# Performance work log

Measured on AMD Instinct MI355X. Metric: run time of the kernel, lower is better.

The kernel has to match this reference:

```python
import jax, jax.numpy as jnp
import numpy as np

BATCH, D_IN, D_HIDDEN, K = 4096, 2048, 16384, 64


def setup_inputs() -> dict:
    key = jax.random.key(0)
    kx, kw = jax.random.split(key)
    x = jax.random.normal(kx, (BATCH, D_IN), dtype=jnp.float32)
    # W init as in the module: randn normalized per column (dim=0) then scaled by 0.1
    W = jax.random.normal(kw, (D_IN, D_HIDDEN), dtype=jnp.float32)
    W = 0.1 * W / jnp.linalg.norm(W, axis=0, keepdims=True)
    b_enc = jnp.zeros((D_HIDDEN,), dtype=jnp.float32)
    b_dec = jnp.zeros((D_IN,), dtype=jnp.float32)
    return {"x": x, "W": W, "b_enc": b_enc, "b_dec": b_dec, "k": K}


def reference(x, W, b_enc, b_dec, k):
    # encode: linear + ReLU
    f = jax.nn.relu(x @ W + b_enc)            # [B, D_HIDDEN]
    # global batch top-k: keep k * batch largest activations across the whole batch
    flat = f.reshape(-1)                      # [B * D_HIDDEN]
    n_keep = k * x.shape[0]                   # static python int
    vals, idx = jax.lax.top_k(flat, n_keep)
    f_topk = jnp.zeros_like(flat).at[idx].set(vals).reshape(f.shape)
    # tied decode
    recon = f_topk @ W.T + b_dec              # [B, D_IN]
    return (recon, f_topk)
```

## Files before the change

### kernel.cpp

```cpp
#include <hip/hip_runtime.h>
#include <stdint.h>


#define BATCH 4096
#define DIN   2048
#define DHID  16384
#define NELEM (BATCH * DHID)
#define RECON_ELEMS (BATCH * DIN)
#define NBINS 8192
#define THRESH_BIN 1664
#define SC_THRESH 0.203125f
#define WIN   3
#define RLCAP 256
#define CBUF2 512
#define NB2 (NBINS - THRESH_BIN)
#define NB2H (NB2 / 2)
#define SCHUNK 32
#define NCH ((NB2 + SCHUNK - 1) / SCHUNK)
#define NKT 32
#define SBUF8 4096
#define WSCALE_INV 0.00390625f

#define XB_OFF   0u
#define HIST_OFF 16777216u
#define META_OFF (HIST_OFF + 32768u)
#define CAND_OFF (HIST_OFF + 65536u)
#define CANDCAP  80000u
#define SC_OFF   18874368u
#define SCCAP    1835008u

#define M_CNT   0
#define M_BLO   1
#define M_BHI   2
#define M_NNEED 3
#define M_NSURE 4
#define M_OVF   5
#define M_SCCNT 6

struct Cand { unsigned long long key; unsigned int idx; float val; };

typedef _Float16 f16x8 __attribute__((ext_vector_type(8)));
typedef float f32x4  __attribute__((ext_vector_type(4)));

__device__ __forceinline__ int binof(float v) {
    int b = (int)(v * 8192.0f);
    return b > (NBINS - 1) ? (NBINS - 1) : b;
}

__device__ __forceinline__ unsigned short f2h(float f) {
    _Float16 h = (_Float16)f;
    return __builtin_bit_cast(unsigned short, h);
}

__device__ __forceinline__ float h2f(unsigned short u) {
    return (float)__builtin_bit_cast(_Float16, u);
}

__device__ __forceinline__ void gload_lds16(const void* g, void* l) {
    __builtin_amdgcn_global_load_lds(
        (const __attribute__((address_space(1))) void*)g,
        (__attribute__((address_space(3))) void*)l, 16, 0, 0);
}

__device__ __forceinline__ void nt_store4(const float4& v, float* p) {
    f32x4 x = {v.x, v.y, v.z, v.w};
    __builtin_nontemporal_store(x, (f32x4*)p);
}

__global__ void init_kernel(unsigned* __restrict__ hist, unsigned* __restrict__ meta) {
    int i = blockIdx.x * 256 + threadIdx.x;
    if (i < NBINS) hist[i] = 0u;
    if (i < 64)    meta[i] = 0u;
}

__global__ __launch_bounds__(256) void prep_kernel(const float* __restrict__ X,
                                                   unsigned short* __restrict__ Xh,
                                                   const float* __restrict__ W,
                                                   float* __restrict__ WT,
                                                   unsigned short* __restrict__ WhT,
                                                   unsigned* __restrict__ hist,
                                                   unsigned* __restrict__ meta,
                                                   unsigned* __restrict__ rowcnt) {
    __shared__ float tile[64][68];
    const int bid = blockIdx.x;
    const int t   = threadIdx.x;
    if (bid < 8192) {
        size_t i = (size_t)bid * 256 + t;
        float4 v = ((const float4*)X)[i];
        ushort4 o;
        o.x = f2h(v.x); o.y = f2h(v.y); o.z = f2h(v.z); o.w = f2h(v.w);
        ((ushort4*)Xh)[i] = o;
        if (bid < 32) {
            int g = bid * 256 + t;
            if (g < NBINS)  hist[g] = 0u;
            if (g < 64)     meta[g] = 0u;
            if (g < BATCH)  rowcnt[g] = 0u;
        }
        return;
    }
    const int bb = bid - 8192;
    const int gx = bb & 255;
    const int gy = bb >> 8;
    const int ra = t >> 4;
    const int ca = (t & 15) * 4;
#pragma unroll
    for (int u = 0; u < 4; ++u) {
        int row = u * 16 + ra;
        float4 v = *(const float4*)&W[(size_t)(gy * 64 + row) * DHID + gx * 64 + ca];
        tile[ca + 0][row] = v.x;
        tile[ca + 1][row] = v.y;
        tile[ca + 2][row] = v.z;
        tile[ca + 3][row] = v.w;
    }
    __syncthreads();
#pragma unroll
    for (int u = 0; u < 4; ++u) {
        int cl = u * 16 + ra;
        float4 v = *(const float4*)&tile[cl][ca];
        size_t o = (size_t)(gx * 64 + cl) * DIN + gy * 64 + ca;
        *(float4*)&WT[o] = v;
        ushort4 b;
        b.x = f2h(v.x * 256.0f); b.y = f2h(v.y * 256.0f);
        b.z = f2h(v.z * 256.0f); b.w = f2h(v.w * 256.0f);
        *(ushort4*)&WhT[o] = b;
    }
}


#define STAGE_A(H, KT) do { if ((KT) < NKT) {                                   \
    const unsigned short* _s = Xh + (size_t)(m0 + (H)*128 + stgrow)*2048        \
                               + (KT)*64 + stgcol;                              \
    unsigned short* _d = lds + ((H)*2 + ((KT)&1))*8192 + stgdst;                \
    gload_lds16(_s, _d);                                                        \
    gload_lds16(_s + 64*2048, _d + 4096);                                       \
} } while (0)

#define STAGE_B(H, KT) do { if ((KT) < NKT) {                                   \
    const unsigned short* _s = WhT + (size_t)(n0 + (H)*128 + stgrow)*2048       \
                               + (KT)*64 + stgcol;                              \
    unsigned short* _d = lds + 32768 + ((H)*2 + ((KT)&1))*8192 + stgdst;        \
    gload_lds16(_s, _d);                                                        \
    gload_lds16(_s + 64*2048, _d + 4096);                                       \
} } while (0)

#define LDA(DST, AH, PAR) do {                                                  \
    _Pragma("unroll")                                                           \
    for (int i = 0; i < 4; ++i) {                                               \
        const unsigned short* _p = lds + ((AH)*2+(PAR))*8192                    \
                                   + (wr2*64 + i*16 + lm)*64;                   \
        DST[i][0] = *(const f16x8*)(_p + cs0);                                  \
        DST[i][1] = *(const f16x8*)(_p + cs1);                                  \
    }                                                                           \
} while (0)

#define LDB(DST, BH, PAR) do {                                                  \
    _Pragma("unroll")                                                           \
    for (int j = 0; j < 2; ++j) {                                               \
        const unsigned short* _p = lds + 32768 + ((BH)*2+(PAR))*8192            \
                                   + (wn*32 + j*16 + lm)*64;                    \
        DST[j][0] = *(const f16x8*)(_p + cs0);                                  \
        DST[j][1] = *(const f16x8*)(_p + cs1);                                  \
    }                                                                           \
} while (0)

#define DO_MFMA(Q, AV, BV) do {                                                 \
    __builtin_amdgcn_s_barrier();                                               \
    asm volatile("s_waitcnt lgkmcnt(0)" ::: "memory");                          \
    __builtin_amdgcn_sched_barrier(0);                                          \
    __builtin_amdgcn_s_setprio(1);                                              \
    _Pragma("unroll")                                                           \
    for (int i = 0; i < 4; ++i)                                                 \
    _Pragma("unroll")                                                           \
    for (int j = 0; j < 2; ++j) {                                               \
        acc[Q][i][j] = __builtin_amdgcn_mfma_f32_16x16x32_f16(                  \
            AV[i][0], BV[j][0], acc[Q][i][j], 0, 0, 0);                         \
        acc[Q][i][j] = __builtin_amdgcn_mfma_f32_16x16x32_f16(                  \
            AV[i][1], BV[j][1], acc[Q][i][j], 0, 0, 0);                         \
    }                                                                           \
    __builtin_amdgcn_s_setprio(0);                                              \
    __builtin_amdgcn_s_barrier();                                               \
    asm volatile("" ::: "memory");                                              \
} while (0)

#define TILE_BODY(PAR, T) do {                                                  \
    LDA(av, 0, PAR); LDB(bv0, 0, PAR);                                          \
    STAGE_B(0, (T) + 1); STAGE_A(1, (T) + 1);                                   \
    DO_MFMA(0, av, bv0);                                                        \
    LDB(bv1, 1, PAR);                                                           \
    DO_MFMA(1, av, bv1);                                                        \
    LDA(av, 1, PAR);                                                            \
    STAGE_A(0, (T) + 2);                                                        \
    DO_MFMA(2, av, bv1);                                                        \
    STAGE_B(1, (T) + 2);                                                        \
    asm volatile("s_waitcnt vmcnt(4)" ::: "memory");                            \
    DO_MFMA(3, av, bv0);                                                        \
} while (0)

__global__ __launch_bounds__(512, 2) void encode_mfma8(const unsigned short* __restrict__ Xh,
                                                       const unsigned short* __restrict__ WhT,
                                                       const float* __restrict__ benc,
                                                       unsigned long long* __restrict__ sc,
                                                       unsigned* __restrict__ meta,
                                                       unsigned* __restrict__ hist,
                                                       float* __restrict__ F) {
    __shared__ unsigned short lds[65536];
    __shared__ unsigned hsh[NB2H];
    __shared__ unsigned s_n, s_base;

    const int t   = threadIdx.x;
    const int wid = t >> 6;
    const int l   = t & 63;
    const int wr2 = wid >> 2;
    const int wn  = wid & 3;
    const int lm  = l & 15;
    const int l7  = l & 7;
    const int cs0 = ((l >> 4) * 8) ^ (l7 * 8);
    const int cs1 = cs0 ^ 32;
    const int stgrow = wid * 8 + (l >> 3);
    const int stgcol = (l7 ^ (l >> 3)) * 8;
    const int stgdst = wid * 512;

    if (t == 0) s_n = 0u;
    for (int i2 = t; i2 < NB2H; i2 += 512) hsh[i2] = 0u;

    const unsigned id  = blockIdx.x;
    const unsigned xcd = id & 7u;
    const unsigned c   = id >> 3;
    const int bx = (int)(xcd * 8u + (c & 7u));
    const int by = (int)(c >> 3);
    const int m0 = by * 256;
    const int n0 = bx * 256;

    f32x4 acc[4][4][2];
#pragma unroll
    for (int q = 0; q < 4; ++q)
#pragma unroll
        for (int i = 0; i < 4; ++i)
#pragma unroll
            for (int j = 0; j < 2; ++j) acc[q][i][j] = (f32x4){0.f, 0.f, 0.f, 0.f};

    STAGE_A(0, 0); STAGE_B(0, 0); STAGE_B(1, 0); STAGE_A(1, 0);
    STAGE_A(0, 1); STAGE_B(1, 1);
    asm volatile("s_waitcnt vmcnt(4)" ::: "memory");
    __builtin_amdgcn_s_barrier();
    asm volatile("" ::: "memory");

    {
        f16x8 av[4][2], bv0[2][2], bv1[2][2];
#pragma unroll 1
        for (int it = 0; it < 16; ++it) {
            const int T = 2 * it;
            TILE_BODY(0, T);
            TILE_BODY(1, T + 1);
        }
    }

    __syncthreads();
    unsigned long long* sbuf = (unsigned long long*)lds;

#pragma unroll
    for (int q = 0; q < 4; ++q) {
        const int qm = (q >= 2) ? 1 : 0;
        const int qn = (q == 1 || q == 2) ? 1 : 0;
#pragma unroll
        for (int j = 0; j < 2; ++j) {
            const int col = n0 + qn * 128 + wn * 32 + j * 16 + lm;
            const float bias = benc[col];
#pragma unroll
            for (int i = 0; i < 4; ++i) {
                const int rbase = m0 + qm * 128 + wr2 * 64 + i * 16 + (l >> 4) * 4;
#pragma unroll
                for (int r = 0; r < 4; ++r) {
                    float v = fmaxf(acc[q][i][j][r] * WSCALE_INV + bias, 0.0f);
                    if (v >= SC_THRESH) {
                        unsigned hx = (unsigned)(binof(v) - THRESH_BIN);
                        atomicAdd(&hsh[hx >> 1], (hx & 1u) ? 65536u : 1u);
                        unsigned flat = (unsigned)(rbase + r) * (unsigned)DHID + (unsigned)col;
                        unsigned long long e =
                            ((unsigned long long)__float_as_uint(v) << 32) | flat;
                        unsigned pos = atomicAdd(&s_n, 1u);
                        if (pos < SBUF8) sbuf[pos] = e;
                        else {
                            unsigned p = atomicAdd(&meta[M_SCCNT], 1u);
                            if (p < SCCAP) sc[p] = e; else meta[M_OVF] = 1u;
                        }
                    }
                }
            }
        }
    }
    {
        const float4 z4 = {0.f, 0.f, 0.f, 0.f};
        const int zr = t >> 6;
        const int zc = (t & 63) * 4;
#pragma unroll 1
        for (int rr = 0; rr < 32; ++rr)
            nt_store4(z4, &F[(size_t)(m0 + zr + rr * 8) * DHID + n0 + zc]);
    }
    __syncthreads();
    unsigned n = s_n < SBUF8 ? s_n : (unsigned)SBUF8;
    if (t == 0) s_base = atomicAdd(&meta[M_SCCNT], n);
    __syncthreads();
    const unsigned base = s_base;
    for (unsigned l2 = t; l2 < n; l2 += 512) {
        unsigned p = base + l2;
        if (p < SCCAP) sc[p] = sbuf[l2]; else meta[M_OVF] = 1u;
    }
    for (int i2 = t; i2 < NB2H; i2 += 512) {
        unsigned u = hsh[i2];
        unsigned lo = u & 0xFFFFu, hi = u >> 16;
        if (lo) atomicAdd(&hist[THRESH_BIN + 2 * i2], lo);
        if (hi) atomicAdd(&hist[THRESH_BIN + 2 * i2 + 1], hi);
    }
}

__global__ void scan_sc(const unsigned* __restrict__ hist,
                        unsigned* __restrict__ meta,
                        const int* __restrict__ kptr) {
    __shared__ unsigned sh[NB2];
    __shared__ unsigned csum[NCH];
    int t = threadIdx.x;
    for (int i = t; i < NB2; i += 256) sh[i] = hist[THRESH_BIN + i];
    __syncthreads();
    if (t < NCH) {
        unsigned s = 0;
        int base = t * SCHUNK;
        for (int u = 0; u < SCHUNK && base + u < NB2; ++u) s += sh[base + u];
        csum[t] = s;
    }
    __syncthreads();
    if (t == 0) {
        unsigned nk = (unsigned)kptr[0] * BATCH;
        unsigned cum = 0;
        int bstar_idx = -1;
        for (int c = NCH - 1; c >= 0; --c) {
            if (cum + csum[c] >= nk) {
                int hi2 = c * SCHUNK + SCHUNK - 1; if (hi2 >= NB2) hi2 = NB2 - 1;
                for (int idx = hi2; idx >= c * SCHUNK; --idx) {
                    cum += sh[idx];
                    if (cum >= nk) { bstar_idx = idx; break; }
                }
                break;
            } else cum += csum[c];
        }
        if (bstar_idx < 0) { meta[M_OVF] = 2u; bstar_idx = WIN; }
        int bstar = THRESH_BIN + bstar_idx;
        int blo = bstar - WIN;
        if (blo < THRESH_BIN) { meta[M_OVF] = 3u; blo = THRESH_BIN; }
        int bhi = bstar + WIN; if (bhi > NBINS - 1) bhi = NBINS - 1;
        int bhi_idx = bhi - THRESH_BIN;
        unsigned nsure = 0;
        int cstart = (bhi_idx + 1 + SCHUNK - 1) / SCHUNK;
        for (int idx = bhi_idx + 1; idx < cstart * SCHUNK && idx < NB2; ++idx) nsure += sh[idx];
        for (int c = cstart; c < NCH; ++c) nsure += csum[c];
        meta[M_BLO]   = (unsigned)blo;
        meta[M_BHI]   = (unsigned)bhi;
        meta[M_NSURE] = nsure;
        meta[M_NNEED] = nk - nsure;
    }
}

__global__ __launch_bounds__(256) void emit_sc(const unsigned long long* __restrict__ sc,
                                               unsigned* __restrict__ meta,
                                               Cand* __restrict__ cand,
                                               unsigned* __restrict__ rowcnt,
                                               unsigned long long* __restrict__ rowlist,
                                               float* __restrict__ F) {
    __shared__ uint2 s_cand[CBUF2];
    __shared__ unsigned s_nc, s_base;
    const int tid = threadIdx.x;
    if (tid == 0) s_nc = 0u;
    __syncthreads();
    const unsigned blo = meta[M_BLO], bhi = meta[M_BHI];
    unsigned C = meta[M_SCCNT]; if (C > SCCAP) C = SCCAP;
    size_t stride = (size_t)gridDim.x * 256;
    for (size_t i = (size_t)blockIdx.x * 256 + tid; i < C; i += stride) {
        unsigned long long e = sc[i];
        unsigned vbits = (unsigned)(e >> 32);
        unsigned idx   = (unsigned)(e & 0xFFFFFFFFu);
        unsigned b = (unsigned)binof(__uint_as_float(vbits));
        if (b > bhi) {
            F[idx] = __uint_as_float(vbits);
            unsigned row = idx >> 14;
            unsigned pos = atomicAdd(&rowcnt[row], 1u);
            if (pos < RLCAP)
                rowlist[(size_t)row * RLCAP + pos] =
                    ((unsigned long long)vbits << 32) | (idx & (DHID - 1));
            else meta[M_OVF] = 1u;
        } else if (b >= blo) {
            unsigned pos = atomicAdd(&s_nc, 1u);
            if (pos < CBUF2) { s_cand[pos].x = idx; s_cand[pos].y = vbits; }
            else {
                unsigned p = atomicAdd(&meta[M_CNT], 1u);
                if (p < CANDCAP) { cand[p].idx = idx; cand[p].val = __uint_as_float(vbits); }
                else meta[M_OVF] = 1u;
            }
        }
    }
    __syncthreads();
    unsigned nc = s_nc < CBUF2 ? s_nc : (unsigned)CBUF2;
    if (tid == 0) s_base = atomicAdd(&meta[M_CNT], nc);
    __syncthreads();
    const unsigned base = s_base;
    for (unsigned l2 = tid; l2 < nc; l2 += 256) {
        unsigned p = base + l2;
        if (p < CANDCAP) { cand[p].idx = s_cand[l2].x; cand[p].val = __uint_as_float(s_cand[l2].y); }
        else meta[M_OVF] = 1u;
    }
}

__global__ __launch_bounds__(256) void exact_wave(const float* __restrict__ X,
                                                  const float* __restrict__ WT,
                                                  const float* __restrict__ benc,
                                                  const unsigned* __restrict__ meta,
                                                  Cand* __restrict__ cand) {
    unsigned C = meta[M_CNT]; if (C > CANDCAP) C = CANDCAP;
    const int lane = threadIdx.x & 63;
    const unsigned wid = blockIdx.x * 4 + (threadIdx.x >> 6);
    const unsigned nw  = gridDim.x * 4;
    for (unsigned c = wid * 2; c < C; c += nw * 2) {
        unsigned c1 = c + 1;
        bool has1 = (c1 < C);
        unsigned idxA = cand[c].idx;
        unsigned idxB = cand[has1 ? c1 : c].idx;
        const float4* xA = (const float4*)(X  + (size_t)(idxA >> 14) * DIN);
        const float4* wA = (const float4*)(WT + (size_t)(idxA & (DHID - 1)) * DIN);
        const float4* xB = (const float4*)(X  + (size_t)(idxB >> 14) * DIN);
        const float4* wB = (const float4*)(WT + (size_t)(idxB & (DHID - 1)) * DIN);
        double a0 = 0.0, a1 = 0.0;
#pragma unroll
        for (int u = 0; u < 8; ++u) {
            float4 xa = xA[lane + 64 * u];
            float4 wa = wA[lane + 64 * u];
            float4 xb = xB[lane + 64 * u];
            float4 wb = wB[lane + 64 * u];
            a0 += (double)xa.x * (double)wa.x + (double)xa.y * (double)wa.y
                + (double)xa.z * (double)wa.z + (double)xa.w * (double)wa.w;
            a1 += (double)xb.x * (double)wb.x + (double)xb.y * (double)wb.y
                + (double)xb.z * (double)wb.z + (double)xb.w * (double)wb.w;
        }
#pragma unroll
        for (int off = 32; off > 0; off >>= 1) {
            a0 += __shfl_down(a0, off, 64);
            a1 += __shfl_down(a1, off, 64);
        }
        if (lane == 0) {
            double v0 = a0 + (double)benc[idxA & (DHID - 1)];
            if (v0 < 0.0) v0 = 0.0;
            cand[c].key = (unsigned long long)__double_as_longlong(v0);
            if (has1) {
                double v1 = a1 + (double)benc[idxB & (DHID - 1)];
                if (v1 < 0.0) v1 = 0.0;
                cand[c1].key = (unsigned long long)__double_as_longlong(v1);
            }
        }
    }
}

__global__ __launch_bounds__(1024) void select_kernel(unsigned* __restrict__ meta,
                                                      Cand* __restrict__ cand) {
    __shared__ unsigned h[4096];
    __shared__ unsigned csum[128];
    __shared__ unsigned long long s_prefix;
    __shared__ unsigned s_need, s_gcnt;
    __shared__ unsigned long long gkey[1024];
    __shared__ unsigned gpos[1024];
    __shared__ unsigned gidx[1024];
    __shared__ unsigned char gkeep[1024];

    int t = threadIdx.x;
    unsigned C = meta[M_CNT]; if (C > CANDCAP) C = CANDCAP;
    if (t == 0) { s_prefix = 0ULL; s_need = meta[M_NNEED]; s_gcnt = 0u; }
    __syncthreads();

    for (int pass = 0; pass < 3; ++pass) {
        for (int i = t; i < 4096; i += 1024) h[i] = 0u;
        __syncthreads();
        int shift = 52 - pass * 12;
        unsigned long long pfx = s_prefix;
        for (unsigned c = t; c < C; c += 1024) {
            unsigned long long key = cand[c].key;
            if (pass == 0 || (key >> (shift + 12)) == pfx)
                atomicAdd(&h[(unsigned)((key >> shift) & 0xFFFULL)], 1u);
        }
        __syncthreads();
        if (t < 128) {
            unsigned s = 0;
#pragma unroll
            for (int u = 0; u < 32; ++u) s += h[t * 32 + u];
            csum[t] = s;
        }
        __syncthreads();
        if (t == 0) {
            unsigned need = s_need;
            unsigned cum2 = 0; int cc = 127;
            for (; cc >= 0; --cc) {
                if (cum2 + csum[cc] >= need) break;
                cum2 += csum[cc];
            }
            int bsel = 0;
            if (cc >= 0) {
                unsigned cum3 = cum2;
                for (int b = cc * 32 + 31; b >= cc * 32; --b) {
                    cum3 += h[b];
                    if (cum3 >= need) { bsel = b; s_need = need - (cum3 - h[b]); break; }
                }
            }
            s_prefix = (s_prefix << 12) | (unsigned long long)bsel;
        }
        __syncthreads();
    }
    unsigned long long pfx = s_prefix;
    for (unsigned c = t; c < C; c += 1024) {
        unsigned long long key = cand[c].key;
        if ((key >> 28) == pfx) {
            unsigned p = atomicAdd(&s_gcnt, 1u);
            if (p < 1024) { gkey[p] = key; gpos[p] = c; gidx[p] = cand[c].idx; gkeep[p] = 0; }
        }
    }
    __syncthreads();
    if (t == 0) {
        unsigned g = s_gcnt < 1024u ? s_gcnt : 1024u;
        unsigned nd = s_need;
        for (unsigned sel = 0; sel < nd && sel < g; ++sel) {
            int best = -1;
            for (unsigned i = 0; i < g; ++i) {
                if (gkeep[i]) continue;
                if (best < 0 || gkey[i] > gkey[best] ||
                    (gkey[i] == gkey[best] && gidx[i] < gidx[best])) best = (int)i;
            }
            if (best >= 0) gkeep[best] = 1;
        }
        for (unsigned i = 0; i < g; ++i)
            if (gkeep[i]) cand[gpos[i]].idx = gidx[i] | 0x80000000u;
    }
    __syncthreads();
    for (unsigned c = t; c < C; c += 1024)
        if ((cand[c].key >> 28) > pfx) cand[c].idx |= 0x80000000u;
}

__global__ __launch_bounds__(256) void restore2_kernel(float* __restrict__ F,
                                                       const unsigned* __restrict__ meta,
                                                       const Cand* __restrict__ cand,
                                                       unsigned* __restrict__ rowcnt,
                                                       unsigned long long* __restrict__ rowlist) {
    unsigned C = meta[M_CNT]; if (C > CANDCAP) C = CANDCAP;
    size_t stride = (size_t)gridDim.x * 256;
    for (size_t c = (size_t)blockIdx.x * 256 + threadIdx.x; c < C; c += stride) {
        unsigned id = cand[c].idx;
        if (id & 0x80000000u) {
            unsigned idx = id & 0x7FFFFFFFu;
            float v = (float)__longlong_as_double((long long)cand[c].key);
            F[idx] = v;
            unsigned row = idx >> 14;
            unsigned j   = idx & (DHID - 1);
            unsigned pos = atomicAdd(&rowcnt[row], 1u);
            if (pos < RLCAP)
                rowlist[(size_t)row * RLCAP + pos] =
                    ((unsigned long long)__float_as_uint(v) << 32) | j;
        }
    }
}

__global__ __launch_bounds__(256) void decode_rl_f32(const unsigned long long* __restrict__ rowlist,
                                                     const unsigned* __restrict__ rowcnt,
                                                     const float* __restrict__ WT,
                                                     const float* __restrict__ bdec,
                                                     float* __restrict__ recon) {
    __shared__ unsigned sj[RLCAP];
    __shared__ float    sv[RLCAP];
    int b = blockIdx.x;
    int t = threadIdx.x;
    unsigned cnt = rowcnt[b]; if (cnt > RLCAP) cnt = RLCAP;
    for (unsigned l = t; l < cnt; l += 256) {
        unsigned long long e = rowlist[(size_t)b * RLCAP + l];
        sj[l] = (unsigned)(e & 0xFFFFFFFFu);
        sv[l] = __uint_as_float((unsigned)(e >> 32));
    }
    __syncthreads();
    float4 acc0 = {0, 0, 0, 0}, acc1 = {0, 0, 0, 0};
    for (unsigned l = 0; l < cnt; ++l) {
        float v = sv[l]; unsigned j = sj[l];
        const float4* w4 = (const float4*)(WT + (size_t)j * DIN);
        float4 wa = w4[t], wb = w4[256 + t];
        acc0.x = fmaf(v, wa.x, acc0.x); acc0.y = fmaf(v, wa.y, acc0.y);
        acc0.z = fmaf(v, wa.z, acc0.z); acc0.w = fmaf(v, wa.w, acc0.w);
        acc1.x = fmaf(v, wb.x, acc1.x); acc1.y = fmaf(v, wb.y, acc1.y);
        acc1.z = fmaf(v, wb.z, acc1.z); acc1.w = fmaf(v, wb.w, acc1.w);
    }
    float4 bd0 = ((const float4*)bdec)[t];
    float4 bd1 = ((const float4*)bdec)[256 + t];
    float4 o0 = {acc0.x + bd0.x, acc0.y + bd0.y, acc0.z + bd0.z, acc0.w + bd0.w};
    float4 o1 = {acc1.x + bd1.x, acc1.y + bd1.y, acc1.z + bd1.z, acc1.w + bd1.w};
    float* dst = recon + (size_t)b * DIN;
    nt_store4(o0, dst + 4 * t);
    nt_store4(o1, dst + 4 * (256 + t));
}

__global__ __launch_bounds__(256) void decode_rl_f16(const unsigned long long* __restrict__ rowlist,
                                                     const unsigned* __restrict__ rowcnt,
                                                     const unsigned short* __restrict__ WhT,
                                                     const float* __restrict__ bdec,
                                                     float* __restrict__ recon) {
    __shared__ unsigned sj[RLCAP];
    __shared__ float    sv[RLCAP];
    int b = blockIdx.x;
    int t = threadIdx.x;
    unsigned cnt = rowcnt[b]; if (cnt > RLCAP) cnt = RLCAP;
    for (unsigned l = t; l < cnt; l += 256) {
        unsigned long long e = rowlist[(size_t)b * RLCAP + l];
        sj[l] = (unsigned)(e & 0xFFFFFFFFu);
        sv[l] = __uint_as_float((unsigned)(e >> 32)) * WSCALE_INV;
    }
    __syncthreads();
    float4 acc0 = {0, 0, 0, 0}, acc1 = {0, 0, 0, 0};
    unsigned l = 0;
    for (; l + 2 <= cnt; l += 2) {
        float v0 = sv[l], v1 = sv[l + 1];
        const ushort4* w0 = (const ushort4*)(WhT + (size_t)sj[l]     * DIN);
        const ushort4* w1 = (const ushort4*)(WhT + (size_t)sj[l + 1] * DIN);
        ushort4 a0 = w0[t], b0 = w0[256 + t];
        ushort4 a1 = w1[t], b1 = w1[256 + t];
        acc0.x = fmaf(v0, h2f(a0.x), acc0.x); acc0.y = fmaf(v0, h2f(a0.y), acc0.y);
        acc0.z = fmaf(v0, h2f(a0.z), acc0.z); acc0.w = fmaf(v0, h2f(a0.w), acc0.w);
        acc1.x = fmaf(v0, h2f(b0.x), acc1.x); acc1.y = fmaf(v0, h2f(b0.y), acc1.y);
        acc1.z = fmaf(v0, h2f(b0.z), acc1.z); acc1.w = fmaf(v0, h2f(b0.w), acc1.w);
        acc0.x = fmaf(v1, h2f(a1.x), acc0.x); acc0.y = fmaf(v1, h2f(a1.y), acc0.y);
        acc0.z = fmaf(v1, h2f(a1.z), acc0.z); acc0.w = fmaf(v1, h2f(a1.w), acc0.w);
        acc1.x = fmaf(v1, h2f(b1.x), acc1.x); acc1.y = fmaf(v1, h2f(b1.y), acc1.y);
        acc1.z = fmaf(v1, h2f(b1.z), acc1.z); acc1.w = fmaf(v1, h2f(b1.w), acc1.w);
    }
    if (l < cnt) {
        float v0 = sv[l];
        const ushort4* w0 = (const ushort4*)(WhT + (size_t)sj[l] * DIN);
        ushort4 a0 = w0[t], b0 = w0[256 + t];
        acc0.x = fmaf(v0, h2f(a0.x), acc0.x); acc0.y = fmaf(v0, h2f(a0.y), acc0.y);
        acc0.z = fmaf(v0, h2f(a0.z), acc0.z); acc0.w = fmaf(v0, h2f(a0.w), acc0.w);
        acc1.x = fmaf(v0, h2f(b0.x), acc1.x); acc1.y = fmaf(v0, h2f(b0.y), acc1.y);
        acc1.z = fmaf(v0, h2f(b0.z), acc1.z); acc1.w = fmaf(v0, h2f(b0.w), acc1.w);
    }
    float4 bd0 = ((const float4*)bdec)[t];
    float4 bd1 = ((const float4*)bdec)[256 + t];
    float4 o0 = {acc0.x + bd0.x, acc0.y + bd0.y, acc0.z + bd0.z, acc0.w + bd0.w};
    float4 o1 = {acc1.x + bd1.x, acc1.y + bd1.y, acc1.z + bd1.z, acc1.w + bd1.w};
    float* dst = recon + (size_t)b * DIN;
    nt_store4(o0, dst + 4 * t);
    nt_store4(o1, dst + 4 * (256 + t));
}

__global__ __launch_bounds__(256) void encode_f32(const float* __restrict__ X,
                                                  const float* __restrict__ W,
                                                  const float* __restrict__ benc,
                                                  float* __restrict__ F) {
    __shared__ float As[16][128];
    __shared__ float Bs[16][128];
    const int t  = threadIdx.x;
    const int n0 = blockIdx.x * 128;
    const int m0 = blockIdx.y * 128;
    const int tx = t & 15, ty = t >> 4;
    const int ra = t >> 1, ca = (t & 1) * 8;
    const int rb = t >> 4, cb = (t & 15) * 8;
    float acc[8][8];
#pragma unroll
    for (int i = 0; i < 8; ++i)
#pragma unroll
        for (int j = 0; j < 8; ++j) acc[i][j] = 0.0f;
    const float* xp = X + (size_t)(m0 + ra) * DIN + ca;
    const float* wp = W + (size_t)rb * DHID + n0 + cb;
    for (int k0 = 0; k0 < DIN; k0 += 16) {
        float4 a0 = *(const float4*)(xp + k0);
        float4 a1 = *(const float4*)(xp + k0 + 4);
        float4 b0 = *(const float4*)(wp + (size_t)k0 * DHID);
        float4 b1 = *(const float4*)(wp + (size_t)k0 * DHID + 4);
        __syncthreads();
        As[ca + 0][ra] = a0.x; As[ca + 1][ra] = a0.y; As[ca + 2][ra] = a0.z; As[ca + 3][ra] = a0.w;
        As[ca + 4][ra] = a1.x; As[ca + 5][ra] = a1.y; As[ca + 6][ra] = a1.z; As[ca + 7][ra] = a1.w;
        *(float4*)&Bs[rb][cb]     = b0;
        *(float4*)&Bs[rb][cb + 4] = b1;
        __syncthreads();
#pragma unroll
        for (int kk = 0; kk < 16; ++kk) {
            float a[8], bb[8];
            *(float4*)&a[0]  = *(const float4*)&As[kk][ty * 8];
            *(float4*)&a[4]  = *(const float4*)&As[kk][ty * 8 + 4];
            *(float4*)&bb[0] = *(const float4*)&Bs[kk][tx * 8];
            *(float4*)&bb[4] = *(const float4*)&Bs[kk][tx * 8 + 4];
#pragma unroll
            for (int i = 0; i < 8; ++i)
#pragma unroll
                for (int j = 0; j < 8; ++j)
                    acc[i][j] = fmaf(a[i], bb[j], acc[i][j]);
        }
    }
    float bias[8];
    *(float4*)&bias[0] = *(const float4*)&benc[n0 + tx * 8];
    *(float4*)&bias[4] = *(const float4*)&benc[n0 + tx * 8 + 4];
#pragma unroll
    for (int i = 0; i < 8; ++i) {
        float out[8];
#pragma unroll
        for (int j = 0; j < 8; ++j) out[j] = fmaxf(acc[i][j] + bias[j], 0.0f);
        float* dst = F + (size_t)(m0 + ty * 8 + i) * DHID + n0 + tx * 8;
        *(float4*)dst       = *(float4*)&out[0];
        *(float4*)(dst + 4) = *(float4*)&out[4];
    }
}

__global__ __launch_bounds__(256) void survey_kernel(const float* __restrict__ F,
                                                     unsigned* __restrict__ hist) {
    __shared__ unsigned h[NBINS];
    for (int i = THRESH_BIN + threadIdx.x; i < NBINS; i += 256) h[i] = 0u;
    __syncthreads();
    const float4* F4 = (const float4*)F;
    size_t stride = (size_t)gridDim.x * 256;
    for (size_t i = (size_t)blockIdx.x * 256 + threadIdx.x; i < NELEM / 4; i += stride) {
        float4 v = F4[i];
        float vv[4] = {v.x, v.y, v.z, v.w};
#pragma unroll
        for (int c = 0; c < 4; ++c) {
            int b = binof(vv[c]);
            if (b >= THRESH_BIN) atomicAdd(&h[b], 1u);
        }
    }
    __syncthreads();
    for (int i2 = THRESH_BIN + threadIdx.x; i2 < NBINS; i2 += 256)
        if (h[i2]) atomicAdd(&hist[i2], h[i2]);
}

__global__ __launch_bounds__(256) void collect_old(const float* __restrict__ F,
                                                   unsigned* __restrict__ meta,
                                                   Cand* __restrict__ cand, unsigned cap) {
    unsigned blo = meta[M_BLO], bhi = meta[M_BHI];
    const float4* F4 = (const float4*)F;
    size_t stride = (size_t)gridDim.x * 256;
    for (size_t i = (size_t)blockIdx.x * 256 + threadIdx.x; i < NELEM / 4; i += stride) {
        float4 v = F4[i];
        float vv[4] = {v.x, v.y, v.z, v.w};
#pragma unroll
        for (int c = 0; c < 4; ++c) {
            unsigned b = (unsigned)binof(vv[c]);
            if (b >= blo && b <= bhi) {
                unsigned p = atomicAdd(&meta[M_CNT], 1u);
                if (p < cap) { cand[p].idx = (unsigned)(i * 4 + c); cand[p].val = vv[c]; }
                else meta[M_OVF] = 1u;
            }
        }
    }
}

__global__ __launch_bounds__(256) void zero_old(float* __restrict__ F,
                                                const unsigned* __restrict__ meta) {
    unsigned bhi = meta[M_BHI];
    float4* F4 = (float4*)F;
    size_t stride = (size_t)gridDim.x * 256;
    for (size_t i = (size_t)blockIdx.x * 256 + threadIdx.x; i < NELEM / 4; i += stride) {
        float4 v = F4[i];
        v.x = ((unsigned)binof(v.x) > bhi) ? v.x : 0.0f;
        v.y = ((unsigned)binof(v.y) > bhi) ? v.y : 0.0f;
        v.z = ((unsigned)binof(v.z) > bhi) ? v.z : 0.0f;
        v.w = ((unsigned)binof(v.w) > bhi) ? v.w : 0.0f;
        F4[i] = v;
    }
}

__global__ __launch_bounds__(256) void exact_old(const float* __restrict__ X,
                                                 const float* __restrict__ W,
                                                 const float* __restrict__ benc,
                                                 const unsigned* __restrict__ meta,
                                                 Cand* __restrict__ cand, unsigned cap) {
    __shared__ double red[256];
    unsigned C = meta[M_CNT]; if (C > cap) C = cap;
    int t = threadIdx.x;
    for (unsigned c = blockIdx.x; c < C; c += gridDim.x) {
        unsigned idx = cand[c].idx;
        int b = (int)(idx >> 14);
        int j = (int)(idx & (DHID - 1));
        const float* xp = X + (size_t)b * DIN + t * 8;
        const float* wp = W + (size_t)(t * 8) * DHID + j;
        double part = 0.0;
#pragma unroll
        for (int u = 0; u < 8; ++u)
            part += (double)xp[u] * (double)wp[(size_t)u * DHID];
        red[t] = part;
        __syncthreads();
        for (int s = 128; s > 0; s >>= 1) {
            if (t < s) red[t] += red[t + s];
            __syncthreads();
        }
        if (t == 0) {
            double v = red[0] + (double)benc[j];
            if (v < 0.0) v = 0.0;
            cand[c].key = (unsigned long long)__double_as_longlong(v);
        }
        __syncthreads();
    }
}

__global__ __launch_bounds__(256) void restore_old(float* __restrict__ F,
                                                   const unsigned* __restrict__ meta,
                                                   const Cand* __restrict__ cand, unsigned cap) {
    unsigned C = meta[M_CNT]; if (C > cap) C = cap;
    size_t stride = (size_t)gridDim.x * 256;
    for (size_t c = (size_t)blockIdx.x * 256 + threadIdx.x; c < C; c += stride) {
        unsigned id = cand[c].idx;
        if (id & 0x80000000u)
            F[id & 0x7FFFFFFFu] = (float)__longlong_as_double((long long)cand[c].key);
    }
}

__global__ __launch_bounds__(256) void decode_old(const float* __restrict__ F,
                                                  const float* __restrict__ W,
                                                  const float* __restrict__ bdec,
                                                  float* __restrict__ recon) {
    __shared__ unsigned sj[4096];
    __shared__ float    sv[4096];
    __shared__ unsigned soff[257];
    int b = blockIdx.x;
    int t = threadIdx.x;
    float4 acc0 = {0, 0, 0, 0}, acc1 = {0, 0, 0, 0};
    const float* frow = F + (size_t)b * DHID;
    for (int seg = 0; seg < 4; ++seg) {
        int base = seg * 4096;
        unsigned cnt = 0;
#pragma unroll
        for (int c = 0; c < 16; ++c)
            if (frow[base + t * 16 + c] != 0.0f) cnt++;
        soff[t] = cnt;
        __syncthreads();
        if (t == 0) {
            unsigned o = 0;
            for (int i = 0; i < 256; ++i) { unsigned tmp = soff[i]; soff[i] = o; o += tmp; }
            soff[256] = o;
        }
        __syncthreads();
        unsigned pos = soff[t];
        for (int c = 0; c < 16; ++c) {
            float v = frow[base + t * 16 + c];
            if (v != 0.0f) { sj[pos] = (unsigned)(base + t * 16 + c); sv[pos] = v; ++pos; }
        }
        __syncthreads();
        unsigned total = soff[256];
        int i0 = t * 4, i1 = 1024 + t * 4;
        for (unsigned l = 0; l < total; ++l) {
            float v = sv[l]; unsigned j = sj[l];
            const float* wp = W + j;
            acc0.x = fmaf(v, wp[(size_t)(i0 + 0) * DHID], acc0.x);
            acc0.y = fmaf(v, wp[(size_t)(i0 + 1) * DHID], acc0.y);
            acc0.z = fmaf(v, wp[(size_t)(i0 + 2) * DHID], acc0.z);
            acc0.w = fmaf(v, wp[(size_t)(i0 + 3) * DHID], acc0.w);
            acc1.x = fmaf(v, wp[(size_t)(i1 + 0) * DHID], acc1.x);
            acc1.y = fmaf(v, wp[(size_t)(i1 + 1) * DHID], acc1.y);
            acc1.z = fmaf(v, wp[(size_t)(i1 + 2) * DHID], acc1.z);
            acc1.w = fmaf(v, wp[(size_t)(i1 + 3) * DHID], acc1.w);
        }
        __syncthreads();
    }
    float4 bd0 = ((const float4*)bdec)[t];
    float4 bd1 = ((const float4*)bdec)[256 + t];
    float4 o0 = {acc0.x + bd0.x, acc0.y + bd0.y, acc0.z + bd0.z, acc0.w + bd0.w};
    float4 o1 = {acc1.x + bd1.x, acc1.y + bd1.y, acc1.z + bd1.z, acc1.w + bd1.w};
    float4* dst = (float4*)(recon + (size_t)b * DIN);
    dst[t]       = o0;
    dst[256 + t] = o1;
}

extern "C" void kernel_launch(void* const* d_in, const int* in_sizes, int n_in,
                              void* d_out, int out_size, void* d_ws, size_t ws_size,
                              hipStream_t stream) {
    const float* X    = (const float*)d_in[0];
    const float* W    = (const float*)d_in[1];
    const float* benc = (const float*)d_in[2];
    const float* bdec = (const float*)d_in[3];
    const int*   kptr = (const int*)d_in[4];

    float* recon = (float*)d_out;
    float* F     = recon + RECON_ELEMS;

    const size_t WT_BYTES  = (size_t)DIN * DHID * sizeof(float);
    const size_t WHT_BYTES = (size_t)DIN * DHID * sizeof(short);
    const size_t ROW_BYTES = 65536 + (size_t)BATCH * RLCAP * 8;
    float* WT = (float*)d_ws;

    if (ws_size >= WT_BYTES + WHT_BYTES) {
        unsigned short* WhT = (unsigned short*)((char*)d_ws + WT_BYTES);
        int f16_decode = (ws_size >= WT_BYTES + WHT_BYTES + ROW_BYTES) ? 1 : 0;
        char* rowbase = f16_decode ? ((char*)d_ws + WT_BYTES + WHT_BYTES)
                                   : ((char*)WhT);
        unsigned* rowcnt = (unsigned*)rowbase;
        unsigned long long* rowlist = (unsigned long long*)(rowbase + 65536);

        unsigned short* Xh = (unsigned short*)((char*)d_out + XB_OFF);
        unsigned* hist = (unsigned*)((char*)d_out + HIST_OFF);
        unsigned* meta = (unsigned*)((char*)d_out + META_OFF);
        Cand*     cand = (Cand*)((char*)d_out + CAND_OFF);
        unsigned long long* sc = (unsigned long long*)((char*)d_out + SC_OFF);

        prep_kernel<<<dim3(16384), dim3(256), 0, stream>>>(X, Xh, W, WT, WhT, hist, meta, rowcnt);
        encode_mfma8<<<dim3(1024), dim3(512), 0, stream>>>(Xh, WhT, benc, sc, meta, hist, F);
        scan_sc<<<dim3(1), dim3(256), 0, stream>>>(hist, meta, kptr);
        emit_sc<<<dim3(512), dim3(256), 0, stream>>>(sc, meta, cand, rowcnt, rowlist, F);
        exact_wave<<<dim3(4096), dim3(256), 0, stream>>>(X, WT, benc, meta, cand);
        select_kernel<<<dim3(1), dim3(1024), 0, stream>>>(meta, cand);
        restore2_kernel<<<dim3(1024), dim3(256), 0, stream>>>(F, meta, cand, rowcnt, rowlist);
        if (f16_decode)
            decode_rl_f16<<<dim3(4096), dim3(256), 0, stream>>>(rowlist, rowcnt, WhT, bdec, recon);
        else
            decode_rl_f32<<<dim3(4096), dim3(256), 0, stream>>>(rowlist, rowcnt, WT, bdec, recon);
    } else {
        unsigned* hist = (unsigned*)d_out;
        unsigned* meta = hist + NBINS;
        Cand*     cand = (Cand*)((char*)d_out + 65536);
        const unsigned cap = 1000000u;

        init_kernel<<<dim3(33), dim3(256), 0, stream>>>(hist, meta);
        encode_f32<<<dim3(128, 32), dim3(256), 0, stream>>>(X, W, benc, F);
        survey_kernel<<<dim3(2048), dim3(256), 0, stream>>>(F, hist);
        scan_sc<<<dim3(1), dim3(256), 0, stream>>>(hist, meta, kptr);
        collect_old<<<dim3(2048), dim3(256), 0, stream>>>(F, meta, cand, cap);
        exact_old<<<dim3(4096), dim3(256), 0, stream>>>(X, W, benc, meta, cand, cap);
        select_kernel<<<dim3(1), dim3(1024), 0, stream>>>(meta, cand);
        zero_old<<<dim3(2048), dim3(256), 0, stream>>>(F, meta);
        restore_old<<<dim3(1024), dim3(256), 0, stream>>>(F, meta, cand, cap);
        decode_old<<<dim3(4096), dim3(256), 0, stream>>>(F, W, bdec, recon);
    }
}
```

Measured before the change: 672.8 us.

## Fuse exact fp64 rescoring of LDS-buffered candidates into emit_sc

Measured after the change: 673.5 us. No clear change (+0.1%).

```diff
diff --git a/kernel.cpp b/kernel.cpp
--- a/kernel.cpp
+++ b/kernel.cpp
@@ -20,6 +20,9 @@
 #define NKT 32
 #define SBUF8 4096
 #define WSCALE_INV 0.00390625f
+#define FLAG_KEY  0x40000000u
+#define FLAG_KEEP 0x80000000u
+#define IDX_MASK  0x3FFFFFFFu
 
 #define XB_OFF   0u
 #define HIST_OFF 16777216u
@@ -65,6 +68,30 @@
 __device__ __forceinline__ void nt_store4(const float4& v, float* p) {
     f32x4 x = {v.x, v.y, v.z, v.w};
     __builtin_nontemporal_store(x, (f32x4*)p);
+}
+
+__device__ __forceinline__ unsigned long long exact_key(const float* __restrict__ X,
+                                                        const float* __restrict__ WT,
+                                                        const float* __restrict__ benc,
+                                                        unsigned idx, int lane) {
+    int b = (int)(idx >> 14);
+    int j = (int)(idx & (DHID - 1));
+    const float4* x4 = (const float4*)(X  + (size_t)b * DIN);
+    const float4* w4 = (const float4*)(WT + (size_t)j * DIN);
+    double acc = 0.0;
+#pragma unroll
+    for (int u = 0; u < 8; ++u) {
+        float4 xv = x4[lane + 64 * u];
+        float4 wv = w4[lane + 64 * u];
+        acc += (double)xv.x * (double)wv.x + (double)xv.y * (double)wv.y
+             + (double)xv.z * (double)wv.z + (double)xv.w * (double)wv.w;
+    }
+#pragma unroll
+    for (int off = 32; off > 0; off >>= 1)
+        acc += __shfl_down(acc, off, 64);
+    double v = acc + (double)benc[j];
+    if (v < 0.0) v = 0.0;
+    return (unsigned long long)__double_as_longlong(v);
 }
 
 __global__ void init_kernel(unsigned* __restrict__ hist, unsigned* __restrict__ meta) {
@@ -365,7 +392,10 @@
                                                Cand* __restrict__ cand,
                                                unsigned* __restrict__ rowcnt,
                                                unsigned long long* __restrict__ rowlist,
-                                               float* __restrict__ F) {
+                                               float* __restrict__ F,
+                                               const float* __restrict__ X,
+                                               const float* __restrict__ WT,
+                                               const float* __restrict__ benc) {
     __shared__ uint2 s_cand[CBUF2];
     __shared__ unsigned s_nc, s_base;
     const int tid = threadIdx.x;
@@ -404,8 +434,56 @@
     const unsigned base = s_base;
     for (unsigned l2 = tid; l2 < nc; l2 += 256) {
         unsigned p = base + l2;
-        if (p < CANDCAP) { cand[p].idx = s_cand[l2].x; cand[p].val = __uint_as_float(s_cand[l2].y); }
-        else meta[M_OVF] = 1u;
+        if (p < CANDCAP) {
+            cand[p].idx = s_cand[l2].x | FLAG_KEY;
+            cand[p].val = __uint_as_float(s_cand[l2].y);
+        } else meta[M_OVF] = 1u;
+    }
+    __syncthreads();
+    const int lane = tid & 63;
+    const int wv   = tid >> 6;
+    for (unsigned cc = (unsigned)wv * 2; cc < nc; cc += 8) {
+        unsigned cc1 = cc + 1;
+        bool has1 = (cc1 < nc);
+        unsigned idxA = s_cand[cc].x;
+        unsigned idxB = s_cand[has1 ? cc1 : cc].x;
+        const float4* xA = (const float4*)(X  + (size_t)(idxA >> 14) * DIN);
+        const float4* wA = (const float4*)(WT + (size_t)(idxA & (DHID - 1)) * DIN);
+        const float4* xB = (const float4*)(X  + (size_t)(idxB >> 14) * DIN);
+        const float4* wB = (const float4*)(WT + (size_t)(idxB & (DHID - 1)) * DIN);
+        double a0 = 0.0, a1 = 0.0;
+#pragma unroll
+        for (int u = 0; u < 8; ++u) {
+            float4 xa = xA[lane + 64 * u];
+            float4 wa = wA[lane + 64 * u];
+            float4 xb = xB[lane + 64 * u];
+            float4 wb = wB[lane + 64 * u];
+            a0 += (double)xa.x * (double)wa.x + (double)xa.y * (double)wa.y
+                + (double)xa.z * (double)wa.z + (double)xa.w * (double)wa.w;
+            a1 += (double)xb.x * (double)wb.x + (double)xb.y * (double)wb.y
+                + (double)xb.z * (double)wb.z + (double)xb.w * (double)wb.w;
+        }
+#pragma unroll
+        for (int off = 32; off > 0; off >>= 1) {
+            a0 += __shfl_down(a0, off, 64);
+            a1 += __shfl_down(a1, off, 64);
+        }
+        if (lane == 0) {
+            unsigned p0 = base + cc;
+            if (p0 < CANDCAP) {
+                double v0 = a0 + (double)benc[idxA & (DHID - 1)];
+                if (v0 < 0.0) v0 = 0.0;
+                cand[p0].key = (unsigned long long)__double_as_longlong(v0);
+            }
+            if (has1) {
+                unsigned p1 = base + cc1;
+                if (p1 < CANDCAP) {
+                    double v1 = a1 + (double)benc[idxB & (DHID - 1)];
+                    if (v1 < 0.0) v1 = 0.0;
+                    cand[p1].key = (unsigned long long)__double_as_longlong(v1);
+                }
+            }
+        }
     }
 }
 
@@ -418,42 +496,10 @@
     const int lane = threadIdx.x & 63;
     const unsigned wid = blockIdx.x * 4 + (threadIdx.x >> 6);
     const unsigned nw  = gridDim.x * 4;
-    for (unsigned c = wid * 2; c < C; c += nw * 2) {
-        unsigned c1 = c + 1;
-        bool has1 = (c1 < C);
-        unsigned idxA = cand[c].idx;
-        unsigned idxB = cand[has1 ? c1 : c].idx;
-        const float4* xA = (const float4*)(X  + (size_t)(idxA >> 14) * DIN);
-        const float4* wA = (const float4*)(WT + (size_t)(idxA & (DHID - 1)) * DIN);
-        const float4* xB = (const float4*)(X  + (size_t)(idxB >> 14) * DIN);
-        const float4* wB = (const float4*)(WT + (size_t)(idxB & (DHID - 1)) * DIN);
-        double a0 = 0.0, a1 = 0.0;
-#pragma unroll
-        for (int u = 0; u < 8; ++u) {
-            float4 xa = xA[lane + 64 * u];
-            float4 wa = wA[lane + 64 * u];
-            float4 xb = xB[lane + 64 * u];
-            float4 wb = wB[lane + 64 * u];
-            a0 += (double)xa.x * (double)wa.x + (double)xa.y * (double)wa.y
-                + (double)xa.z * (double)wa.z + (double)xa.w * (double)wa.w;
-            a1 += (double)xb.x * (double)wb.x + (double)xb.y * (double)wb.y
-                + (double)xb.z * (double)wb.z + (double)xb.w * (double)wb.w;
-        }
-#pragma unroll
-        for (int off = 32; off > 0; off >>= 1) {
-            a0 += __shfl_down(a0, off, 64);
-            a1 += __shfl_down(a1, off, 64);
-        }
-        if (lane == 0) {
-            double v0 = a0 + (double)benc[idxA & (DHID - 1)];
-            if (v0 < 0.0) v0 = 0.0;
-            cand[c].key = (unsigned long long)__double_as_longlong(v0);
-            if (has1) {
-                double v1 = a1 + (double)benc[idxB & (DHID - 1)];
-                if (v1 < 0.0) v1 = 0.0;
-                cand[c1].key = (unsigned long long)__double_as_longlong(v1);
-            }
-        }
+    for (unsigned c = wid; c < C; c += nw) {
+        unsigned id = cand[c].idx;
+        if (id & FLAG_KEY) continue;
+        cand[c].key = exact_key(X, WT, benc, id & IDX_MASK, lane);
     }
 }
 
@@ -515,7 +561,11 @@
         unsigned long long key = cand[c].key;
         if ((key >> 28) == pfx) {
             unsigned p = atomicAdd(&s_gcnt, 1u);
-            if (p < 1024) { gkey[p] = key; gpos[p] = c; gidx[p] = cand[c].idx; gkeep[p] = 0; }
+            if (p < 1024) {
+                gkey[p] = key; gpos[p] = c;
+                gidx[p] = cand[c].idx & IDX_MASK;
+                gkeep[p] = 0;
+            }
         }
     }
     __syncthreads();
@@ -532,11 +582,11 @@
             if (best >= 0) gkeep[best] = 1;
         }
         for (unsigned i = 0; i < g; ++i)
-            if (gkeep[i]) cand[gpos[i]].idx = gidx[i] | 0x80000000u;
+            if (gkeep[i]) cand[gpos[i]].idx = gidx[i] | FLAG_KEEP;
     }
     __syncthreads();
     for (unsigned c = t; c < C; c += 1024)
-        if ((cand[c].key >> 28) > pfx) cand[c].idx |= 0x80000000u;
+        if ((cand[c].key >> 28) > pfx) cand[c].idx |= FLAG_KEEP;
 }
 
 __global__ __launch_bounds__(256) void restore2_kernel(float* __restrict__ F,
@@ -548,8 +598,8 @@
     size_t stride = (size_t)gridDim.x * 256;
     for (size_t c = (size_t)blockIdx.x * 256 + threadIdx.x; c < C; c += stride) {
         unsigned id = cand[c].idx;
-        if (id & 0x80000000u) {
-            unsigned idx = id & 0x7FFFFFFFu;
+        if (id & FLAG_KEEP) {
+            unsigned idx = id & IDX_MASK;
             float v = (float)__longlong_as_double((long long)cand[c].key);
             F[idx] = v;
             unsigned row = idx >> 14;
@@ -803,8 +853,8 @@
     size_t stride = (size_t)gridDim.x * 256;
     for (size_t c = (size_t)blockIdx.x * 256 + threadIdx.x; c < C; c += stride) {
         unsigned id = cand[c].idx;
-        if (id & 0x80000000u)
-            F[id & 0x7FFFFFFFu] = (float)__longlong_as_double((long long)cand[c].key);
+        if (id & FLAG_KEEP)
+            F[id & IDX_MASK] = (float)__longlong_as_double((long long)cand[c].key);
     }
 }
 
@@ -898,8 +948,8 @@
         prep_kernel<<<dim3(16384), dim3(256), 0, stream>>>(X, Xh, W, WT, WhT, hist, meta, rowcnt);
         encode_mfma8<<<dim3(1024), dim3(512), 0, stream>>>(Xh, WhT, benc, sc, meta, hist, F);
         scan_sc<<<dim3(1), dim3(256), 0, stream>>>(hist, meta, kptr);
-        emit_sc<<<dim3(512), dim3(256), 0, stream>>>(sc, meta, cand, rowcnt, rowlist, F);
-        exact_wave<<<dim3(4096), dim3(256), 0, stream>>>(X, WT, benc, meta, cand);
+        emit_sc<<<dim3(2048), dim3(256), 0, stream>>>(sc, meta, cand, rowcnt, rowlist, F, X, WT, benc);
+        exact_wave<<<dim3(1024), dim3(256), 0, stream>>>(X, WT, benc, meta, cand);
         select_kernel<<<dim3(1), dim3(1024), 0, stream>>>(meta, cand);
         restore2_kernel<<<dim3(1024), dim3(256), 0, stream>>>(F, meta, cand, rowcnt, rowlist);
         if (f16_decode)
```
